# Kernel tuning notes

Measured on AMD Instinct MI355X. Metric: run time of the kernel, lower is better.

## Reference

```python
import jax, jax.numpy as jnp
import numpy as np

B = 16
TOP_N = 4
IOU_THRESH = 0.25
PAD = 224
OUT = 224  # part image size
NUM_CLASSES = 200


def _gen_anchors(input_shape=(448, 448)):
    # Faithful port of NTSNet._generate_default_anchor_maps -> edge anchors,
    # then +PAD shift and int cast as in NTSNet.__init__.
    scales = [2.0 ** (1.0 / 3.0), 2.0 ** (2.0 / 3.0)]
    ratios = [0.667, 1.0, 1.5]
    settings = [(32, 48, scales), (64, 96, scales), (128, 192, [1.0] + scales)]
    edge = []
    for stride, size, scs in settings:
        H = int(np.ceil(input_shape[0] / stride))
        W = int(np.ceil(input_shape[1] / stride))
        ostart = stride / 2.0
        oy = np.arange(ostart, ostart + stride * H, stride).reshape(H, 1)
        ox = np.arange(ostart, ostart + stride * W, stride).reshape(1, W)
        cy = np.broadcast_to(oy, (H, W)).astype(np.float32)
        cx = np.broadcast_to(ox, (H, W)).astype(np.float32)
        for s in scs:
            for ar in ratios:
                h = size * s / float(ar) ** 0.5
                w = size * s * float(ar) ** 0.5
                e = np.stack([cy - h / 2.0, cx - w / 2.0, cy + h / 2.0, cx + w / 2.0], axis=-1)
                edge.append(e.reshape(-1, 4))
    edge = np.concatenate(edge, axis=0).astype(np.float32)
    return (edge + PAD).astype(np.int64).astype(np.int32)  # [1614,4] (y0,x0,y1,x1)


def _conv(x, w, b, stride, pad):
    y = jax.lax.conv_general_dilated(
        x, w, window_strides=(stride, stride),
        padding=[(pad, pad), (pad, pad)],
        dimension_numbers=("NCHW", "OIHW", "NCHW"))
    return y + b[None, :, None, None]


def _nms_single(scores, boxes, areas):
    # Hard NMS, fixed TOP_N iterations (jit-friendly): iteratively take the
    # highest-score box and suppress boxes with IoU >= IOU_THRESH.
    valid = jnp.ones(scores.shape, dtype=bool)
    picked = []
    for _ in range(TOP_N):
        i = jnp.argmax(jnp.where(valid, scores, -jnp.inf))
        b = boxes[i]
        ih = jnp.minimum(boxes[:, 2], b[2]) - jnp.maximum(boxes[:, 0], b[0])
        iw = jnp.minimum(boxes[:, 3], b[3]) - jnp.maximum(boxes[:, 1], b[1])
        inter = jnp.where((ih < 0) | (iw < 0), 0.0, ih * iw)
        iou = inter / (areas + areas[i] - inter)
        valid = valid & (iou < IOU_THRESH)
        picked.append(i)
    return jnp.stack(picked)  # [TOP_N]


def _crop_resize(img, box):
    # Bilinear resize of img[:, y0:y1, x0:x1] to OUTxOUT, align_corners=True
    # (matches F.interpolate(..., mode='bilinear', align_corners=True)).
    y0, x0, y1, x1 = box[0], box[1], box[2], box[3]
    h = (y1 - y0).astype(jnp.float32)
    w = (x1 - x0).astype(jnp.float32)
    t = jnp.arange(OUT, dtype=jnp.float32)
    sy = t * (h - 1.0) / (OUT - 1.0)
    sx = t * (w - 1.0) / (OUT - 1.0)
    fy = jnp.floor(sy)
    fx = jnp.floor(sx)
    wy = (sy - fy)[None, :, None]  # broadcast over rows
    wx = (sx - fx)[None, None, :]  # broadcast over cols
    iy0 = y0 + fy.astype(jnp.int32)
    ix0 = x0 + fx.astype(jnp.int32)
    iy1 = jnp.minimum(iy0 + 1, y1 - 1)
    ix1 = jnp.minimum(ix0 + 1, x1 - 1)
    r0 = img[:, iy0]  # [3,OUT,896]
    r1 = img[:, iy1]
    top = r0[:, :, ix0] * (1.0 - wx) + r0[:, :, ix1] * wx
    bot = r1[:, :, ix0] * (1.0 - wx) + r1[:, :, ix1] * wx
    return top * (1.0 - wy) + bot * wy  # [3,OUT,OUT]


def setup_inputs() -> dict:
    key = jax.random.key(0)
    ks = jax.random.split(key, 10)
    s = 0.02
    inp = {
        "x": jax.random.normal(ks[0], (B, 3, 448, 448), jnp.float32),
        "bb_w": jax.random.normal(ks[1], (2048, 3, 32, 32), jnp.float32) * s,
        "bb_b": jnp.zeros((2048,), jnp.float32),
        "n1_dw": jax.random.normal(ks[2], (128, 2048, 3, 3), jnp.float32) * s,
        "n1_db": jnp.zeros((128,), jnp.float32),
        "n1_tw": jax.random.normal(ks[3], (6, 128, 1, 1), jnp.float32) * s,
        "n1_tb": jnp.zeros((6,), jnp.float32),
        "n2_dw": jax.random.normal(ks[4], (128, 128, 3, 3), jnp.float32) * s,
        "n2_db": jnp.zeros((128,), jnp.float32),
        "n2_tw": jax.random.normal(ks[5], (6, 128, 1, 1), jnp.float32) * s,
        "n2_tb": jnp.zeros((6,), jnp.float32),
        "n3_dw": jax.random.normal(ks[6], (128, 128, 3, 3), jnp.float32) * s,
        "n3_db": jnp.zeros((128,), jnp.float32),
        "n3_tw": jax.random.normal(ks[7], (9, 128, 1, 1), jnp.float32) * s,
        "n3_tb": jnp.zeros((9,), jnp.float32),
        "cn_w": jax.random.normal(ks[8], (NUM_CLASSES, 10240), jnp.float32) * s,
        "cn_b": jnp.zeros((NUM_CLASSES,), jnp.float32),
        "anchors": jnp.asarray(_gen_anchors()),
    }
    return inp


def reference(x, bb_w, bb_b, n1_dw, n1_db, n1_tw, n1_tb, n2_dw, n2_db, n2_tw,
              n2_tb, n3_dw, n3_db, n3_tw, n3_tb, cn_w, cn_b, anchors):
    batch = x.shape[0]
    # Backbone -> raw pre-features [B,2048,14,14]
    raw = _conv(x, bb_w, bb_b, stride=32, pad=0)
    # Navigator unit -> rpn scores [B,1614]
    y1 = jax.nn.relu(_conv(raw, n1_dw, n1_db, 1, 1))            # [B,128,14,14]
    t1 = _conv(y1, n1_tw, n1_tb, 1, 0).reshape(batch, -1)        # [B,1176]
    y2 = jax.nn.relu(_conv(y1, n2_dw, n2_db, 2, 1))              # [B,128,7,7]
    t2 = _conv(y2, n2_tw, n2_tb, 1, 0).reshape(batch, -1)        # [B,294]
    y3 = jax.nn.relu(_conv(y2, n3_dw, n3_db, 2, 1))              # [B,128,4,4]
    t3 = _conv(y3, n3_tw, n3_tb, 1, 0).reshape(batch, -1)        # [B,144]
    rpn_score = jnp.concatenate([t1, t2, t3], axis=1)            # [B,1614]

    boxes_f = anchors.astype(jnp.float32)
    areas = (boxes_f[:, 2] - boxes_f[:, 0]) * (boxes_f[:, 3] - boxes_f[:, 1])
    top_idx = jax.vmap(_nms_single, in_axes=(0, None, None))(rpn_score, boxes_f, areas)  # [B,TOP_N]

    x_pad = jnp.pad(x, ((0, 0), (0, 0), (PAD, PAD), (PAD, PAD)))  # [B,3,896,896]
    sel_boxes = anchors[top_idx]                                  # [B,TOP_N,4]
    part_imgs = jax.vmap(lambda img, bs: jax.vmap(_crop_resize, in_axes=(None, 0))(img, bs))(
        x_pad, sel_boxes)                                         # [B,TOP_N,3,224,224]
    part_imgs = jax.lax.stop_gradient(part_imgs).reshape(batch * TOP_N, 3, OUT, OUT)

    # Shared backbone + tail (global avg pool; dropout is identity in eval)
    part_features = _conv(part_imgs, bb_w, bb_b, 32, 0).mean(axis=(2, 3))  # [B*TOP_N,2048]
    part_feature = part_features.reshape(batch, TOP_N, -1)[:, :4].reshape(batch, -1)  # num_cat=4
    raw_features = jax.lax.stop_gradient(raw).mean(axis=(2, 3))            # [B,2048]

    concat_out = jnp.concatenate([part_feature, raw_features], axis=1)     # [B,10240]
    concat_logits = concat_out @ cn_w.T + cn_b
    return concat_logits
```

## Files before the change

### kernel.cpp

```cpp
#include <hip/hip_runtime.h>
#include <cstdint>
#include <math.h>

typedef _Float16 half_t;
typedef __attribute__((ext_vector_type(8))) _Float16 half8;
typedef __attribute__((ext_vector_type(4))) float floatx4;


typedef __attribute__((address_space(3))) unsigned int lds_u32;
typedef const __attribute__((address_space(1))) unsigned int glb_u32;
__device__ __forceinline__ void glds16(const void* g, void* l) {
    __builtin_amdgcn_global_load_lds((glb_u32*)g, (lds_u32*)l, 16, 0, 0);
}

__global__ __launch_bounds__(256)
void prep_all(const float* __restrict__ x, const float* __restrict__ bbw,
              const float* __restrict__ n1dw, const float* __restrict__ n2dw,
              const float* __restrict__ n3dw, const float* __restrict__ cnb,
              const float* __restrict__ bbb,
              half_t* __restrict__ xh,
              half_t* __restrict__ bh, half_t* __restrict__ w1h,
              float* __restrict__ wt2t, float* __restrict__ wt3t,
              float* __restrict__ out, float* __restrict__ zpad,
              float* __restrict__ concat)
{
    const int t = blockIdx.x * 256 + threadIdx.x;
    if (t < 307200) {
        const int m = t % 3200, s = t / 3200;
        const int mt = m >> 7, mr = m & 127;
        float f[32];
        if (m < 3136) {
            const int bq = m / 196, pos = m % 196, oy = pos / 14, ox = pos % 14;
            const int c = s >> 5, r = s & 31;
            const float* p = x + ((size_t)(bq * 3 + c) * 448 + oy * 32 + r) * 448 + ox * 32;
            #pragma unroll
            for (int i = 0; i < 8; ++i) *(float4*)&f[i * 4] = *(const float4*)(p + i * 4);
        } else {
            #pragma unroll
            for (int j = 0; j < 32; ++j) f[j] = 0.f;
        }
        #pragma unroll
        for (int kg = 0; kg < 4; ++kg) {
            half8 h;
            #pragma unroll
            for (int j = 0; j < 8; ++j) h[j] = (half_t)f[kg * 8 + j];
            const size_t dst = (((size_t)(mt * 96 + s) * 4 + kg) * 128 + mr) * 8;
            *(half8*)(xh + dst) = h;
        }
    } else if (t < 503808) {
        const int t2 = t - 307200;
        const int n = t2 & 2047, s = t2 >> 11;
        const float* p = bbw + (size_t)n * 3072 + s * 32;
        float f[32];
        #pragma unroll
        for (int i = 0; i < 8; ++i) *(float4*)&f[i * 4] = *(const float4*)(p + i * 4);
        const int nt = n >> 6, nr = n & 63;
        #pragma unroll
        for (int kg = 0; kg < 4; ++kg) {
            half8 h;
            #pragma unroll
            for (int j = 0; j < 8; ++j) h[j] = (half_t)f[kg * 8 + j];
            const size_t dst = (((size_t)(nt * 96 + s) * 4 + kg) * 64 + nr) * 8;
            *(half8*)(bh + dst) = h;
        }
    } else if (t < 536576) {
        const int t2 = t - 503808;
        const int n = t2 >> 8, ic8 = t2 & 255;
        const int s = ic8 >> 2, kg = ic8 & 3;
        const float* src = n1dw + ((size_t)n * 2048 + ic8 * 8) * 9;
        float buf[72];
        #pragma unroll
        for (int i = 0; i < 18; ++i) *(float4*)&buf[i * 4] = *(const float4*)(src + i * 4);
        #pragma unroll
        for (int tap = 0; tap < 9; ++tap) {
            half8 h;
            #pragma unroll
            for (int j = 0; j < 8; ++j) h[j] = (half_t)buf[j * 9 + tap];
            const size_t dst = (((size_t)(tap * 64 + s) * 4 + kg) * 128 + n) * 8;
            *(half8*)(w1h + dst) = h;
        }
    } else if (t < 684032) {
        const int t2 = t - 536576;
        const int oc = t2 % 128, rest = t2 / 128, ic = rest % 128, tap = rest / 128;
        wt2t[(tap * 128 + ic) * 128 + oc] = n2dw[((size_t)oc * 128 + ic) * 9 + tap];
    } else if (t < 831488) {
        const int t2 = t - 684032;
        const int oc = t2 % 128, rest = t2 / 128, ic = rest % 128, tap = rest / 128;
        wt3t[(tap * 128 + ic) * 128 + oc] = n3dw[((size_t)oc * 128 + ic) * 9 + tap];
    } else if (t < 834688) {
        const int i = t - 831488;
        out[i] = cnb[i % 200];
    } else if (t < 834944) {
        zpad[t - 834688] = 0.f;
    } else if (t < 998784) {
        const int i = t - 834944;
        const int r = i % 10240;
        concat[i] = (r < 8192) ? bbb[r & 2047] : 0.f;
    }
}

__global__ __launch_bounds__(256)
void gemm_x(const half_t* __restrict__ Ah, const half_t* __restrict__ Bh,
            const float* __restrict__ bias, half_t* __restrict__ outh)
{
    __shared__ __align__(16) char L[32768];
    const int tid = threadIdx.x, lane = tid & 63, wv = tid >> 6;
    const int nt = blockIdx.x, mt = blockIdx.y;
    const int lm = lane & 15, quad = lane >> 4;

    const char* pA = (const char*)Ah + (size_t)(mt >> 1) * 786432 + (mt & 1) * 1024
                   + quad * 2048 + (wv * 16 + lm) * 16;
    const char* gB = (const char*)Bh + (size_t)(2 * nt) * 393216 + lane * 16;

    const int bsi = wv >> 1, bnh = wv & 1;
    const size_t bgb = (size_t)bnh * 393216 + bsi * 4096;
    const int blb = (bsi * 2 + bnh) * 4096;

    floatx4 acc[8];
    const floatx4 fz = {0.f, 0.f, 0.f, 0.f};
    #pragma unroll
    for (int j = 0; j < 8; ++j) acc[j] = fz;

    half8 aC0, aC1, aN0, aN1;

    #pragma unroll
    for (int i = 0; i < 4; ++i)
        glds16(gB + bgb + i * 1024, L + blb + i * 1024);
    aC0 = *(const half8*)(pA);
    aC1 = *(const half8*)(pA + 8192);

    auto step = [&](int s, int sn, const char* Lc, char* Ln,
                    half8& c0, half8& c1, half8& n0, half8& n1) {
        #pragma unroll
        for (int i = 0; i < 4; ++i)
            glds16(gB + bgb + (size_t)sn * 8192 + i * 1024, Ln + blb + i * 1024);
        n0 = *(const half8*)(pA + (size_t)sn * 16384);
        n1 = *(const half8*)(pA + (size_t)sn * 16384 + 8192);
        asm volatile("s_waitcnt vmcnt(6)" ::: "memory");
        __builtin_amdgcn_s_barrier();
        __builtin_amdgcn_sched_barrier(0);
        #pragma unroll
        for (int ki = 0; ki < 2; ++ki) {
            const half8 a = ki ? c1 : c0;
            #pragma unroll
            for (int j = 0; j < 8; ++j) {
                half8 b = *(const half8*)(Lc + (ki * 2 + (j >> 2)) * 4096 + quad * 1024 + ((j & 3) * 16 + lm) * 16);
                acc[j] = __builtin_amdgcn_mfma_f32_16x16x32_f16(a, b, acc[j], 0, 0, 0);
            }
        }
        __builtin_amdgcn_sched_barrier(0);
        __builtin_amdgcn_s_barrier();
    };

    for (int h = 0; h < 24; ++h) {
        const int s0 = 2 * h, s1 = 2 * h + 1;
        step(s0, s0 + 1, L, L + 16384, aC0, aC1, aN0, aN1);
        step(s1, (s1 < 47) ? s1 + 1 : 0, L + 16384, L, aN0, aN1, aC0, aC1);
    }

    const int m0 = mt * 64 + wv * 16 + quad * 4;
    #pragma unroll
    for (int j = 0; j < 8; ++j) {
        const int n = nt * 128 + j * 16 + lm;
        const float bv = bias[n];
        #pragma unroll
        for (int r = 0; r < 4; ++r)
            outh[(size_t)(m0 + r) * 2048 + n] = (half_t)(acc[j][r] + bv);
    }
}

__global__ __launch_bounds__(256)
void gemm_nav(const half_t* __restrict__ rawh, const half_t* __restrict__ Bh,
              const char* __restrict__ zpad, float* __restrict__ y1p)
{
    __shared__ __align__(16) char L[32768];
    const int tid = threadIdx.x, lane = tid & 63, wv = tid >> 6;
    const int tx = blockIdx.x;
    const int tap = tx >> 1, ks = tx & 1;
    const int mt = blockIdx.y;
    const int lm = lane & 15, quad = lane >> 4;

    const int grow = mt * 64 + wv * 16 + lm;
    const int b = grow / 196, pos = grow % 196, oy = pos / 14, ox = pos % 14;
    const int iy = oy + tap / 3 - 1, ix = ox + tap % 3 - 1;
    const bool av = (iy >= 0 && iy < 14 && ix >= 0 && ix < 14);
    const char* fb = av ? (const char*)rawh + ((size_t)(b * 196 + iy * 14 + ix)) * 4096 + ks * 2048 : zpad;
    const int fstp = av ? 1 : 0;
    const char* fbase = fb + fstp * quad * 16;

    const int bsi = wv >> 1, bnh = wv & 1;
    const char* gB = (const char*)Bh + (size_t)tap * 524288 + (size_t)(ks * 32) * 8192 + bnh * 1024 + lane * 16;
    const int blb = bsi * 8192 + bnh * 1024;

    floatx4 acc[8];
    const floatx4 fz = {0.f, 0.f, 0.f, 0.f};
    #pragma unroll
    for (int j = 0; j < 8; ++j) acc[j] = fz;

    half8 aC0, aC1, aN0, aN1;

    #pragma unroll
    for (int i = 0; i < 4; ++i)
        glds16(gB + (size_t)bsi * 8192 + i * 2048, L + blb + i * 2048);
    aC0 = *(const half8*)(fbase);
    aC1 = *(const half8*)(fbase + fstp * 64);

    auto step = [&](int s, int sn, const char* Lc, char* Ln,
                    half8& c0, half8& c1, half8& n0, half8& n1) {
        #pragma unroll
        for (int i = 0; i < 4; ++i)
            glds16(gB + (size_t)(2 * sn + bsi) * 8192 + i * 2048, Ln + blb + i * 2048);
        n0 = *(const half8*)(fbase + fstp * (sn * 128));
        n1 = *(const half8*)(fbase + fstp * (sn * 128 + 64));
        asm volatile("s_waitcnt vmcnt(6)" ::: "memory");
        __builtin_amdgcn_s_barrier();
        __builtin_amdgcn_sched_barrier(0);
        #pragma unroll
        for (int ki = 0; ki < 2; ++ki) {
            const half8 a = ki ? c1 : c0;
            #pragma unroll
            for (int j = 0; j < 8; ++j) {
                half8 bq = *(const half8*)(Lc + ki * 8192 + quad * 2048 + (j * 16 + lm) * 16);
                acc[j] = __builtin_amdgcn_mfma_f32_16x16x32_f16(a, bq, acc[j], 0, 0, 0);
            }
        }
        __builtin_amdgcn_sched_barrier(0);
        __builtin_amdgcn_s_barrier();
    };

    for (int h = 0; h < 8; ++h) {
        const int s0 = 2 * h, s1 = 2 * h + 1;
        step(s0, s0 + 1, L, L + 16384, aC0, aC1, aN0, aN1);
        step(s1, (s1 < 15) ? s1 + 1 : 0, L + 16384, L, aN0, aN1, aC0, aC1);
    }

    const int m0 = mt * 64 + wv * 16 + quad * 4;
    #pragma unroll
    for (int j = 0; j < 8; ++j) {
        const int n = j * 16 + lm;
        #pragma unroll
        for (int r = 0; r < 4; ++r)
            y1p[((size_t)tx * 3136 + m0 + r) * 128 + n] = acc[j][r];
    }
}

__global__ __launch_bounds__(256)
void y1r_rm(const float* __restrict__ y1p, const float* __restrict__ bias,
            float* __restrict__ y1,
            const half_t* __restrict__ rh, float* __restrict__ concat)
{
    if (blockIdx.x < 1568) {
        const int t = blockIdx.x * 256 + threadIdx.x;
        const int n = t & 127;
        float s = bias[n];
        #pragma unroll
        for (int ks = 0; ks < 18; ++ks) s += y1p[(size_t)ks * 3136 * 128 + t];
        y1[t] = fmaxf(s, 0.f);
    } else {
        const int t = (blockIdx.x - 1568) * 256 + threadIdx.x;
        const int n = t & 2047, b = (t >> 11) & 15, pc = t >> 15;
        float s = 0.f;
        const int p0 = pc * 49;
        for (int p = p0; p < p0 + 49; ++p)
            s += (float)rh[(size_t)(b * 196 + p) * 2048 + n];
        atomicAdd(concat + (size_t)b * 10240 + 8192 + n, s * (1.f / 196.f));
    }
}

__device__ __forceinline__ void tidy_one(const float* in, const float* wr, float bi,
                                         float* dst, int lane)
{
    float acc = in[lane] * wr[lane] + in[lane + 64] * wr[lane + 64];
    #pragma unroll
    for (int s = 32; s > 0; s >>= 1) acc += __shfl_down(acc, s, 64);
    if (lane == 0) *dst = acc + bi;
}

__device__ __forceinline__ void conv_s2_body(int t, const float* __restrict__ in,
                                             const float* __restrict__ wt,
                                             const float* __restrict__ bias,
                                             float* __restrict__ out, int Win, int Wout)
{
    const int oc = t & 127;
    const int pos = (t >> 7) % (Wout * Wout);
    const int b = t / (128 * Wout * Wout);
    if (b >= 16) return;
    const int oy = pos / Wout, ox = pos % Wout;
    float acc = bias[oc];
    for (int dy = 0; dy < 3; ++dy) {
        const int y = oy * 2 + dy - 1;
        if (y < 0 || y >= Win) continue;
        for (int dx = 0; dx < 3; ++dx) {
            const int x = ox * 2 + dx - 1;
            if (x < 0 || x >= Win) continue;
            const float* ip = in + (size_t)(b * Win * Win + y * Win + x) * 128;
            const float* wp = wt + (size_t)(dy * 3 + dx) * 16384 + oc;
            for (int ic = 0; ic < 128; ++ic)
                acc += ip[ic] * wp[ic * 128];
        }
    }
    out[(size_t)(b * Wout * Wout + pos) * 128 + oc] = fmaxf(acc, 0.f);
}

__global__ __launch_bounds__(256)
void conv2_tidy1(const float* __restrict__ y1, const float* __restrict__ wt2t,
                 const float* __restrict__ b2d, float* __restrict__ y2,
                 const float* __restrict__ w1t, const float* __restrict__ b1t,
                 float* __restrict__ scores)
{
    if (blockIdx.x < 392) {
        conv_s2_body(blockIdx.x * 256 + threadIdx.x, y1, wt2t, b2d, y2, 14, 7);
    } else {
        const int wid = (blockIdx.x - 392) * 4 + (threadIdx.x >> 6);
        const int lane = threadIdx.x & 63;
        if (wid >= 16 * 1176) return;
        const int b = wid / 1176, i1 = wid % 1176;
        const int ch = i1 / 196, pos = i1 % 196;
        tidy_one(y1 + (size_t)(b * 196 + pos) * 128, w1t + ch * 128, b1t[ch],
                 scores + b * 1614 + i1, lane);
    }
}

__global__ __launch_bounds__(256)
void conv3_tidy2(const float* __restrict__ y2, const float* __restrict__ wt3t,
                 const float* __restrict__ b3d, float* __restrict__ y3,
                 const float* __restrict__ w2t, const float* __restrict__ b2t,
                 float* __restrict__ scores)
{
    if (blockIdx.x < 128) {
        conv_s2_body(blockIdx.x * 256 + threadIdx.x, y2, wt3t, b3d, y3, 7, 4);
    } else {
        const int wid = (blockIdx.x - 128) * 4 + (threadIdx.x >> 6);
        const int lane = threadIdx.x & 63;
        if (wid >= 16 * 294) return;
        const int b = wid / 294, i2 = wid % 294;
        const int ch = i2 / 49, pos = i2 % 49;
        tidy_one(y2 + (size_t)(b * 49 + pos) * 128, w2t + ch * 128, b2t[ch],
                 scores + b * 1614 + 1176 + i2, lane);
    }
}

__global__ __launch_bounds__(256)
void tidy3(const float* __restrict__ y3, const float* __restrict__ w3t,
           const float* __restrict__ b3t, float* __restrict__ scores)
{
    const int wid = blockIdx.x * 4 + (threadIdx.x >> 6);
    const int lane = threadIdx.x & 63;
    if (wid >= 16 * 144) return;
    const int b = wid / 144, i3 = wid % 144;
    const int ch = i3 / 16, pos = i3 % 16;
    tidy_one(y3 + (size_t)(b * 16 + pos) * 128, w3t + ch * 128, b3t[ch],
             scores + b * 1614 + 1470 + i3, lane);
}

__global__ __launch_bounds__(256)
void nms(const float* __restrict__ scores, const int* __restrict__ anchors,
         int* __restrict__ top_idx)
{
    __shared__ float wv_v[4];
    __shared__ int wv_i[4];
    __shared__ int s_pick;
    const int b = blockIdx.x, tid = threadIdx.x;
    const int lane = tid & 63, wv = tid >> 6;
    float sc[7], ay0[7], ax0[7], ay1[7], ax1[7];
    unsigned int vmask = 0;
    #pragma unroll
    for (int j = 0; j < 7; ++j) {
        const int i = tid + j * 256;
        if (i < 1614) {
            sc[j]  = scores[b * 1614 + i];
            ay0[j] = (float)anchors[i * 4 + 0];
            ax0[j] = (float)anchors[i * 4 + 1];
            ay1[j] = (float)anchors[i * 4 + 2];
            ax1[j] = (float)anchors[i * 4 + 3];
            vmask |= 1u << j;
        }
    }
    for (int r = 0; r < 4; ++r) {
        float bv = -INFINITY; int bi = 0x7fffffff;
        #pragma unroll
        for (int j = 0; j < 7; ++j) {
            if (vmask & (1u << j)) {
                const float v = sc[j];
                const int i = tid + j * 256;
                if (v > bv || (v == bv && i < bi)) { bv = v; bi = i; }
            }
        }
        #pragma unroll
        for (int s = 32; s > 0; s >>= 1) {
            const float v2 = __shfl_down(bv, s, 64);
            const int   i2 = __shfl_down(bi, s, 64);
            if (v2 > bv || (v2 == bv && i2 < bi)) { bv = v2; bi = i2; }
        }
        if (lane == 0) { wv_v[wv] = bv; wv_i[wv] = bi; }
        __syncthreads();
        if (tid == 0) {
            float fv = wv_v[0]; int fi = wv_i[0];
            #pragma unroll
            for (int k = 1; k < 4; ++k)
                if (wv_v[k] > fv || (wv_v[k] == fv && wv_i[k] < fi)) { fv = wv_v[k]; fi = wv_i[k]; }
            s_pick = fi;
            top_idx[b * 4 + r] = fi;
        }
        __syncthreads();
        const int pick = s_pick;
        const float py0 = (float)anchors[pick * 4 + 0], px0 = (float)anchors[pick * 4 + 1];
        const float py1 = (float)anchors[pick * 4 + 2], px1 = (float)anchors[pick * 4 + 3];
        const float pa = (py1 - py0) * (px1 - px0);
        #pragma unroll
        for (int j = 0; j < 7; ++j) {
            if (vmask & (1u << j)) {
                const float ih = fminf(ay1[j], py1) - fmaxf(ay0[j], py0);
                const float iw = fminf(ax1[j], px1) - fmaxf(ax0[j], px0);
                const float inter = (ih < 0.f || iw < 0.f) ? 0.f : ih * iw;
                const float area = (ay1[j] - ay0[j]) * (ax1[j] - ax0[j]);
                const float iou = inter / ((area + pa) - inter);
                if (iou >= 0.25f) vmask &= ~(1u << j);
            }
        }
    }
}

__global__ __launch_bounds__(256)
void crop_mean(const float* __restrict__ x, const int* __restrict__ anchors,
               const int* __restrict__ top_idx, float* __restrict__ abar)
{
    __shared__ float red[256];
    const int bi = blockIdx.x;
    const int q = bi / 96, rem = bi % 96, c = rem >> 5, r = rem & 31;
    const int tid = threadIdx.x;
    const int cc = tid & 31, ps = tid >> 5;
    const int idx = top_idx[q];
    const int y0 = anchors[idx * 4 + 0], x0 = anchors[idx * 4 + 1];
    const int y1 = anchors[idx * 4 + 2], x1 = anchors[idx * 4 + 3];
    const float hh = (float)(y1 - y0), ww = (float)(x1 - x0);
    const float* xb = x + (size_t)((q >> 2) * 3 + c) * 200704;
    float acc = 0.f;
    for (int p = ps; p < 49; p += 8) {
        const int oy = p / 7, ox = p % 7;
        const int typ = oy * 32 + r;
        const int txp = ox * 32 + cc;
        const float sy = (float)typ * (hh - 1.0f) / 223.0f;
        const float fy = floorf(sy);
        const float wy = sy - fy;
        const int iy0 = y0 + (int)fy;
        const int iy1 = min(iy0 + 1, y1 - 1);
        const float sx = (float)txp * (ww - 1.0f) / 223.0f;
        const float fx = floorf(sx);
        const float wx = sx - fx;
        const int ix0 = x0 + (int)fx;
        const int ix1 = min(ix0 + 1, x1 - 1);
        const int ry0 = iy0 - 224, ry1 = iy1 - 224;
        const int rx0 = ix0 - 224, rx1 = ix1 - 224;
        const bool vy0 = (ry0 >= 0 && ry0 < 448), vy1 = (ry1 >= 0 && ry1 < 448);
        const bool vx0 = (rx0 >= 0 && rx0 < 448), vx1 = (rx1 >= 0 && rx1 < 448);
        const float v00 = (vy0 && vx0) ? xb[(size_t)ry0 * 448 + rx0] : 0.f;
        const float v01 = (vy0 && vx1) ? xb[(size_t)ry0 * 448 + rx1] : 0.f;
        const float v10 = (vy1 && vx0) ? xb[(size_t)ry1 * 448 + rx0] : 0.f;
        const float v11 = (vy1 && vx1) ? xb[(size_t)ry1 * 448 + rx1] : 0.f;
        const float top = v00 * (1.f - wx) + v01 * wx;
        const float bot = v10 * (1.f - wx) + v11 * wx;
        acc += top * (1.f - wy) + bot * wy;
    }
    red[tid] = acc;
    __syncthreads();
    if (tid < 32) {
        float s = 0.f;
        #pragma unroll
        for (int k = 0; k < 8; ++k) s += red[tid + 32 * k];
        abar[(size_t)q * 3072 + c * 1024 + r * 32 + cc] = s * (1.f / 49.f);
    }
}

__global__ __launch_bounds__(256)
void part_gemm(const float* __restrict__ abar, const half_t* __restrict__ Bh,
               float* __restrict__ concat)
{
    __shared__ __align__(16) char L[12288];
    const int tid = threadIdx.x, lane = tid & 63, wv = tid >> 6;
    const int lm = lane & 15, quad = lane >> 4;
    const int nt = blockIdx.x, ks = blockIdx.y;
    const char* gBh = (const char*)Bh + ((size_t)nt * 96 + ks * 12) * 4096 + lane * 16;
    const int am = tid & 63, akg = tid >> 6;

    floatx4 acc[4], accl[4];
    const floatx4 fz = {0.f, 0.f, 0.f, 0.f};
    #pragma unroll
    for (int j = 0; j < 4; ++j) { acc[j] = fz; accl[j] = fz; }

    for (int s = 0; s < 12; ++s) {
        {
            const float* pa = abar + (size_t)am * 3072 + (ks * 12 + s) * 32 + akg * 8;
            float f[8];
            *(float4*)&f[0] = *(const float4*)pa;
            *(float4*)&f[4] = *(const float4*)(pa + 4);
            half8 h, l;
            #pragma unroll
            for (int j = 0; j < 8; ++j) {
                const half_t hh = (half_t)f[j];
                h[j] = hh;
                l[j] = (half_t)(f[j] - (float)hh);
            }
            *(half8*)(L + (akg * 64 + am) * 16) = h;
            *(half8*)(L + 4096 + (akg * 64 + am) * 16) = l;
        }
        glds16(gBh + (size_t)s * 4096 + wv * 1024, L + 8192 + wv * 1024);
        __syncthreads();
        half8 ah, al, bh[4];
        ah = *(const half8*)(L + (quad * 64 + wv * 16 + lm) * 16);
        al = *(const half8*)(L + 4096 + (quad * 64 + wv * 16 + lm) * 16);
        #pragma unroll
        for (int j = 0; j < 4; ++j) bh[j] = *(const half8*)(L + 8192 + (quad * 64 + j * 16 + lm) * 16);
        #pragma unroll
        for (int j = 0; j < 4; ++j) {
            acc[j]  = __builtin_amdgcn_mfma_f32_16x16x32_f16(ah, bh[j], acc[j], 0, 0, 0);
            accl[j] = __builtin_amdgcn_mfma_f32_16x16x32_f16(al, bh[j], accl[j], 0, 0, 0);
        }
        __syncthreads();
    }
    #pragma unroll
    for (int j = 0; j < 4; ++j) {
        const int n = nt * 64 + j * 16 + lm;
        #pragma unroll
        for (int r = 0; r < 4; ++r) {
            const int m = wv * 16 + quad * 4 + r;
            atomicAdd(concat + (size_t)(m >> 2) * 10240 + (m & 3) * 2048 + n,
                      acc[j][r] + accl[j][r]);
        }
    }
}

__global__ __launch_bounds__(256)
void cls_gemm(const float* __restrict__ concat, const float* __restrict__ w,
              float* __restrict__ out)
{
    __shared__ float ws_[8 * 321];
    __shared__ float cs_[16 * 321];
    __shared__ float red[256];
    const int nchunk = blockIdx.x, ks = blockIdx.y;
    const int tid = threadIdx.x;
    for (int i = tid; i < 2560; i += 256) {
        const int r = i / 320, k = i % 320;
        ws_[r * 321 + k] = w[(size_t)(nchunk * 8 + r) * 10240 + ks * 320 + k];
    }
    for (int i = tid; i < 5120; i += 256) {
        const int r = i / 320, k = i % 320;
        cs_[r * 321 + k] = concat[(size_t)r * 10240 + ks * 320 + k];
    }
    __syncthreads();
    const int b = tid & 15, c = (tid >> 4) & 7, hf = tid >> 7;
    const float* cp = cs_ + b * 321 + hf * 160;
    const float* wp = ws_ + c * 321 + hf * 160;
    float a = 0.f;
    #pragma unroll 8
    for (int k = 0; k < 160; ++k) a += cp[k] * wp[k];
    red[tid] = a;
    __syncthreads();
    if (tid < 128) atomicAdd(out + b * 200 + nchunk * 8 + c, red[tid] + red[tid + 128]);
}

extern "C" void kernel_launch(void* const* d_in, const int* in_sizes, int n_in,
                              void* d_out, int out_size, void* d_ws, size_t ws_size,
                              hipStream_t stream)
{
    const float* x     = (const float*)d_in[0];
    const float* bb_w  = (const float*)d_in[1];
    const float* bb_b  = (const float*)d_in[2];
    const float* n1_dw = (const float*)d_in[3];
    const float* n1_db = (const float*)d_in[4];
    const float* n1_tw = (const float*)d_in[5];
    const float* n1_tb = (const float*)d_in[6];
    const float* n2_dw = (const float*)d_in[7];
    const float* n2_db = (const float*)d_in[8];
    const float* n2_tw = (const float*)d_in[9];
    const float* n2_tb = (const float*)d_in[10];
    const float* n3_dw = (const float*)d_in[11];
    const float* n3_db = (const float*)d_in[12];
    const float* n3_tw = (const float*)d_in[13];
    const float* n3_tb = (const float*)d_in[14];
    const float* cn_w  = (const float*)d_in[15];
    const float* cn_b  = (const float*)d_in[16];
    const int*   anchors = (const int*)d_in[17];
    float* out = (float*)d_out;
    char* W = (char*)d_ws;

    half_t* bbwh  = (half_t*)(W + 0);
    float*  zpad  = (float*)(W + 12582912);
    int*    topidx= (int*)(W + 12583936);
    float*  scores= (float*)(W + 12584960);
    float*  y1    = (float*)(W + 12688384);
    float*  y2    = (float*)(W + 14294016);
    float*  y3    = (float*)(W + 14695424);
    float*  concat= (float*)(W + 14826496);
    half_t* w1h   = (half_t*)(W + 15481856);
    float*  wt2t  = (float*)(W + 20200448);
    float*  wt3t  = (float*)(W + 20790272);
    char* E = W + 21380096;
    half_t* xh    = (half_t*)E;
    float*  y1p   = (float*)E;
    char* F = W + 60701696;
    half_t* rawh  = (half_t*)F;
    float*  abar  = (float*)F;

    prep_all<<<3902, 256, 0, stream>>>(x, bb_w, n1_dw, n2_dw, n3_dw, cn_b, bb_b,
                                       xh, bbwh, w1h, wt2t, wt3t, out, zpad, concat);

    gemm_x<<<dim3(16, 49), 256, 0, stream>>>(xh, bbwh, bb_b, rawh);
    gemm_nav<<<dim3(18, 49), 256, 0, stream>>>(rawh, w1h, (const char*)zpad, y1p);
    y1r_rm<<<2080, 256, 0, stream>>>(y1p, n1_db, y1, rawh, concat);

    conv2_tidy1<<<5096, 256, 0, stream>>>(y1, wt2t, n2_db, y2, n1_tw, n1_tb, scores);
    conv3_tidy2<<<1304, 256, 0, stream>>>(y2, wt3t, n3_db, y3, n2_tw, n2_tb, scores);
    tidy3<<<576, 256, 0, stream>>>(y3, n3_tw, n3_tb, scores);

    nms<<<16, 256, 0, stream>>>(scores, anchors, topidx);
    crop_mean<<<6144, 256, 0, stream>>>(x, anchors, topidx, abar);

    part_gemm<<<dim3(32, 8), 256, 0, stream>>>(abar, bbwh, concat);
    cls_gemm<<<dim3(25, 32), 256, 0, stream>>>(concat, cn_w, out);
}
```

Baseline: 380.5 us.

## Switch backbone and navigator GEMMs to 32x32x16 MFMA with 2x2 wave tiling

Both the feature GEMM and the navigator conv GEMM move from 16x16x32 MFMA with each wave owning 16 rows by 128 columns to 32x32x16 MFMA with a 2x2 wave grid, each wave owning a 32x64 output tile. This cuts LDS reads of B per MFMA and reduces the MFMA instruction count for the same work. The cost is four A fragments in flight per step instead of two, an adjusted vmcnt wait, and a new output-store index mapping that must match the 32x32 accumulator layout.

```diff
diff --git a/kernel.cpp b/kernel.cpp
--- a/kernel.cpp
+++ b/kernel.cpp
@@ -5,6 +5,7 @@
 typedef _Float16 half_t;
 typedef __attribute__((ext_vector_type(8))) _Float16 half8;
 typedef __attribute__((ext_vector_type(4))) float floatx4;
+typedef __attribute__((ext_vector_type(16))) float floatx16;
 
 
 typedef __attribute__((address_space(3))) unsigned int lds_u32;
@@ -105,67 +106,78 @@
 {
     __shared__ __align__(16) char L[32768];
     const int tid = threadIdx.x, lane = tid & 63, wv = tid >> 6;
-    const int nt = blockIdx.x, mt = blockIdx.y;
-    const int lm = lane & 15, quad = lane >> 4;
-
-    const char* pA = (const char*)Ah + (size_t)(mt >> 1) * 786432 + (mt & 1) * 1024
-                   + quad * 2048 + (wv * 16 + lm) * 16;
+    const int nt = blockIdx.x, mt2 = blockIdx.y;
+    const int l31 = lane & 31, hi = lane >> 5;
+    const int wr = wv >> 1, wc = wv & 1;
+
+    const int mr = (mt2 & 1) * 64 + wr * 32 + l31;
+    const char* gA = (const char*)Ah + (size_t)(mt2 >> 1) * 786432 + (size_t)hi * 2048 + mr * 16;
+
     const char* gB = (const char*)Bh + (size_t)(2 * nt) * 393216 + lane * 16;
-
     const int bsi = wv >> 1, bnh = wv & 1;
     const size_t bgb = (size_t)bnh * 393216 + bsi * 4096;
     const int blb = (bsi * 2 + bnh) * 4096;
 
-    floatx4 acc[8];
-    const floatx4 fz = {0.f, 0.f, 0.f, 0.f};
-    #pragma unroll
-    for (int j = 0; j < 8; ++j) acc[j] = fz;
-
-    half8 aC0, aC1, aN0, aN1;
+    const int brd = wc * 4096 + hi * 1024 + l31 * 16;
+
+    floatx16 acc0 = {0.f}, acc1 = {0.f};
+    #pragma unroll
+    for (int r = 0; r < 16; ++r) { acc0[r] = 0.f; acc1[r] = 0.f; }
+
+    half8 aC0, aC1, aC2, aC3, aN0, aN1, aN2, aN3;
 
     #pragma unroll
     for (int i = 0; i < 4; ++i)
         glds16(gB + bgb + i * 1024, L + blb + i * 1024);
-    aC0 = *(const half8*)(pA);
-    aC1 = *(const half8*)(pA + 8192);
-
-    auto step = [&](int s, int sn, const char* Lc, char* Ln,
-                    half8& c0, half8& c1, half8& n0, half8& n1) {
+    aC0 = *(const half8*)(gA);
+    aC1 = *(const half8*)(gA + 4096);
+    aC2 = *(const half8*)(gA + 8192);
+    aC3 = *(const half8*)(gA + 12288);
+
+    auto step = [&](int sn, const char* Lc, char* Ln,
+                    half8& c0, half8& c1, half8& c2, half8& c3,
+                    half8& n0, half8& n1, half8& n2, half8& n3) {
         #pragma unroll
         for (int i = 0; i < 4; ++i)
             glds16(gB + bgb + (size_t)sn * 8192 + i * 1024, Ln + blb + i * 1024);
-        n0 = *(const half8*)(pA + (size_t)sn * 16384);
-        n1 = *(const half8*)(pA + (size_t)sn * 16384 + 8192);
-        asm volatile("s_waitcnt vmcnt(6)" ::: "memory");
+        const char* pAs = gA + (size_t)sn * 16384;
+        n0 = *(const half8*)(pAs);
+        n1 = *(const half8*)(pAs + 4096);
+        n2 = *(const half8*)(pAs + 8192);
+        n3 = *(const half8*)(pAs + 12288);
+        asm volatile("s_waitcnt vmcnt(8)" ::: "memory");
         __builtin_amdgcn_s_barrier();
         __builtin_amdgcn_sched_barrier(0);
         #pragma unroll
-        for (int ki = 0; ki < 2; ++ki) {
-            const half8 a = ki ? c1 : c0;
-            #pragma unroll
-            for (int j = 0; j < 8; ++j) {
-                half8 b = *(const half8*)(Lc + (ki * 2 + (j >> 2)) * 4096 + quad * 1024 + ((j & 3) * 16 + lm) * 16);
-                acc[j] = __builtin_amdgcn_mfma_f32_16x16x32_f16(a, b, acc[j], 0, 0, 0);
-            }
+        for (int t = 0; t < 4; ++t) {
+            const half8 a = (t == 0) ? c0 : (t == 1) ? c1 : (t == 2) ? c2 : c3;
+            const char* bb = Lc + (t >> 1) * 8192 + (t & 1) * 2048 + brd;
+            half8 b0 = *(const half8*)(bb);
+            half8 b1 = *(const half8*)(bb + 512);
+            acc0 = __builtin_amdgcn_mfma_f32_32x32x16_f16(a, b0, acc0, 0, 0, 0);
+            acc1 = __builtin_amdgcn_mfma_f32_32x32x16_f16(a, b1, acc1, 0, 0, 0);
         }
         __builtin_amdgcn_sched_barrier(0);
         __builtin_amdgcn_s_barrier();
     };
 
     for (int h = 0; h < 24; ++h) {
-        const int s0 = 2 * h, s1 = 2 * h + 1;
-        step(s0, s0 + 1, L, L + 16384, aC0, aC1, aN0, aN1);
-        step(s1, (s1 < 47) ? s1 + 1 : 0, L + 16384, L, aN0, aN1, aC0, aC1);
-    }
-
-    const int m0 = mt * 64 + wv * 16 + quad * 4;
-    #pragma unroll
-    for (int j = 0; j < 8; ++j) {
-        const int n = nt * 128 + j * 16 + lm;
+        const int s1 = 2 * h + 1;
+        step(s1, L, L + 16384, aC0, aC1, aC2, aC3, aN0, aN1, aN2, aN3);
+        step((s1 < 47) ? s1 + 1 : 0, L + 16384, L, aN0, aN1, aN2, aN3, aC0, aC1, aC2, aC3);
+    }
+
+    const int m0 = mt2 * 64 + wr * 32 + 4 * hi;
+    #pragma unroll
+    for (int c = 0; c < 2; ++c) {
+        const int n = nt * 128 + wc * 64 + c * 32 + l31;
         const float bv = bias[n];
-        #pragma unroll
-        for (int r = 0; r < 4; ++r)
-            outh[(size_t)(m0 + r) * 2048 + n] = (half_t)(acc[j][r] + bv);
+        const floatx16 av = c ? acc1 : acc0;
+        #pragma unroll
+        for (int r = 0; r < 16; ++r) {
+            const int row = m0 + (r & 3) + 8 * (r >> 2);
+            outh[(size_t)row * 2048 + n] = (half_t)(av[r] + bv);
+        }
     }
 }
 
@@ -178,69 +190,80 @@
     const int tx = blockIdx.x;
     const int tap = tx >> 1, ks = tx & 1;
     const int mt = blockIdx.y;
-    const int lm = lane & 15, quad = lane >> 4;
-
-    const int grow = mt * 64 + wv * 16 + lm;
+    const int l31 = lane & 31, hi = lane >> 5;
+    const int wr = wv >> 1, wc = wv & 1;
+
+    const int grow = mt * 64 + wr * 32 + l31;
     const int b = grow / 196, pos = grow % 196, oy = pos / 14, ox = pos % 14;
     const int iy = oy + tap / 3 - 1, ix = ox + tap % 3 - 1;
     const bool av = (iy >= 0 && iy < 14 && ix >= 0 && ix < 14);
     const char* fb = av ? (const char*)rawh + ((size_t)(b * 196 + iy * 14 + ix)) * 4096 + ks * 2048 : zpad;
     const int fstp = av ? 1 : 0;
-    const char* fbase = fb + fstp * quad * 16;
+    const char* fbase = fb + fstp * (hi * 16);
 
     const int bsi = wv >> 1, bnh = wv & 1;
     const char* gB = (const char*)Bh + (size_t)tap * 524288 + (size_t)(ks * 32) * 8192 + bnh * 1024 + lane * 16;
     const int blb = bsi * 8192 + bnh * 1024;
 
-    floatx4 acc[8];
-    const floatx4 fz = {0.f, 0.f, 0.f, 0.f};
-    #pragma unroll
-    for (int j = 0; j < 8; ++j) acc[j] = fz;
-
-    half8 aC0, aC1, aN0, aN1;
+    const int brd = hi * 2048 + wc * 1024 + l31 * 16;
+
+    floatx16 acc0, acc1;
+    #pragma unroll
+    for (int r = 0; r < 16; ++r) { acc0[r] = 0.f; acc1[r] = 0.f; }
+
+    half8 aC0, aC1, aC2, aC3, aN0, aN1, aN2, aN3;
 
     #pragma unroll
     for (int i = 0; i < 4; ++i)
         glds16(gB + (size_t)bsi * 8192 + i * 2048, L + blb + i * 2048);
     aC0 = *(const half8*)(fbase);
-    aC1 = *(const half8*)(fbase + fstp * 64);
-
-    auto step = [&](int s, int sn, const char* Lc, char* Ln,
-                    half8& c0, half8& c1, half8& n0, half8& n1) {
+    aC1 = *(const half8*)(fbase + fstp * 32);
+    aC2 = *(const half8*)(fbase + fstp * 64);
+    aC3 = *(const half8*)(fbase + fstp * 96);
+
+    auto step = [&](int sn, const char* Lc, char* Ln,
+                    half8& c0, half8& c1, half8& c2, half8& c3,
+                    half8& n0, half8& n1, half8& n2, half8& n3) {
         #pragma unroll
         for (int i = 0; i < 4; ++i)
             glds16(gB + (size_t)(2 * sn + bsi) * 8192 + i * 2048, Ln + blb + i * 2048);
-        n0 = *(const half8*)(fbase + fstp * (sn * 128));
-        n1 = *(const half8*)(fbase + fstp * (sn * 128 + 64));
-        asm volatile("s_waitcnt vmcnt(6)" ::: "memory");
+        const char* pAs = fbase + fstp * (sn * 128);
+        n0 = *(const half8*)(pAs);
+        n1 = *(const half8*)(pAs + fstp * 32);
+        n2 = *(const half8*)(pAs + fstp * 64);
+        n3 = *(const half8*)(pAs + fstp * 96);
+        asm volatile("s_waitcnt vmcnt(8)" ::: "memory");
         __builtin_amdgcn_s_barrier();
         __builtin_amdgcn_sched_barrier(0);
         #pragma unroll
-        for (int ki = 0; ki < 2; ++ki) {
-            const half8 a = ki ? c1 : c0;
-            #pragma unroll
-            for (int j = 0; j < 8; ++j) {
-                half8 bq = *(const half8*)(Lc + ki * 8192 + quad * 2048 + (j * 16 + lm) * 16);
-                acc[j] = __builtin_amdgcn_mfma_f32_16x16x32_f16(a, bq, acc[j], 0, 0, 0);
-            }
+        for (int t = 0; t < 4; ++t) {
+            const half8 a = (t == 0) ? c0 : (t == 1) ? c1 : (t == 2) ? c2 : c3;
+            const char* bb = Lc + (t >> 1) * 8192 + (t & 1) * 4096 + brd;
+            half8 b0 = *(const half8*)(bb);
+            half8 b1 = *(const half8*)(bb + 512);
+            acc0 = __builtin_amdgcn_mfma_f32_32x32x16_f16(a, b0, acc0, 0, 0, 0);
+            acc1 = __builtin_amdgcn_mfma_f32_32x32x16_f16(a, b1, acc1, 0, 0, 0);
         }
         __builtin_amdgcn_sched_barrier(0);
         __builtin_amdgcn_s_barrier();
     };
 
     for (int h = 0; h < 8; ++h) {
-        const int s0 = 2 * h, s1 = 2 * h + 1;
-        step(s0, s0 + 1, L, L + 16384, aC0, aC1, aN0, aN1);
-        step(s1, (s1 < 15) ? s1 + 1 : 0, L + 16384, L, aN0, aN1, aC0, aC1);
-    }
-
-    const int m0 = mt * 64 + wv * 16 + quad * 4;
-    #pragma unroll
-    for (int j = 0; j < 8; ++j) {
-        const int n = j * 16 + lm;
-        #pragma unroll
-        for (int r = 0; r < 4; ++r)
-            y1p[((size_t)tx * 3136 + m0 + r) * 128 + n] = acc[j][r];
+        const int s1 = 2 * h + 1;
+        step(s1, L, L + 16384, aC0, aC1, aC2, aC3, aN0, aN1, aN2, aN3);
+        step((s1 < 15) ? s1 + 1 : 0, L + 16384, L, aN0, aN1, aN2, aN3, aC0, aC1, aC2, aC3);
+    }
+
+    const int m0 = mt * 64 + wr * 32 + 4 * hi;
+    #pragma unroll
+    for (int c = 0; c < 2; ++c) {
+        const int n = wc * 64 + c * 32 + l31;
+        const floatx16 avv = c ? acc1 : acc0;
+        #pragma unroll
+        for (int r = 0; r < 16; ++r) {
+            const int row = m0 + (r & 3) + 8 * (r >> 2);
+            y1p[((size_t)tx * 3136 + row) * 128 + n] = avv[r];
+        }
     }
 }
 
```

Result: slower. 401.6 us (+5.5%).

## Use two-wave blocks with 32-row per-wave tiles in backbone and nav GEMMs

Applied to the files above, without the earlier changes.

Both MFMA GEMM kernels now launch 128 threads instead of 256. Each wave computes two 16-row M subtiles against the same B fragments read from LDS, so every LDS B load feeds two MFMAs. Each wave now issues 8 global-to-LDS copies per step and 4 A-register loads, with the waitcnt adjusted to match. This raises per-wave register use and halves the waves per block, which may reduce latency hiding and occupancy while cutting LDS read traffic per MFMA.

```diff
diff --git a/kernel.cpp b/kernel.cpp
--- a/kernel.cpp
+++ b/kernel.cpp
@@ -99,7 +99,7 @@
     }
 }
 
-__global__ __launch_bounds__(256)
+__global__ __launch_bounds__(128)
 void gemm_x(const half_t* __restrict__ Ah, const half_t* __restrict__ Bh,
             const float* __restrict__ bias, half_t* __restrict__ outh)
 {
@@ -108,44 +108,52 @@
     const int nt = blockIdx.x, mt = blockIdx.y;
     const int lm = lane & 15, quad = lane >> 4;
 
-    const char* pA = (const char*)Ah + (size_t)(mt >> 1) * 786432 + (mt & 1) * 1024
-                   + quad * 2048 + (wv * 16 + lm) * 16;
+    const char* pA = (const char*)Ah + (size_t)(mt >> 1) * 786432
+                   + quad * 2048 + ((mt & 1) * 64 + wv * 32 + lm) * 16;
     const char* gB = (const char*)Bh + (size_t)(2 * nt) * 393216 + lane * 16;
 
-    const int bsi = wv >> 1, bnh = wv & 1;
-    const size_t bgb = (size_t)bnh * 393216 + bsi * 4096;
-    const int blb = (bsi * 2 + bnh) * 4096;
-
-    floatx4 acc[8];
+    floatx4 acc[2][8];
     const floatx4 fz = {0.f, 0.f, 0.f, 0.f};
     #pragma unroll
-    for (int j = 0; j < 8; ++j) acc[j] = fz;
-
-    half8 aC0, aC1, aN0, aN1;
-
-    #pragma unroll
-    for (int i = 0; i < 4; ++i)
-        glds16(gB + bgb + i * 1024, L + blb + i * 1024);
-    aC0 = *(const half8*)(pA);
-    aC1 = *(const half8*)(pA + 8192);
-
-    auto step = [&](int s, int sn, const char* Lc, char* Ln,
-                    half8& c0, half8& c1, half8& n0, half8& n1) {
-        #pragma unroll
-        for (int i = 0; i < 4; ++i)
-            glds16(gB + bgb + (size_t)sn * 8192 + i * 1024, Ln + blb + i * 1024);
-        n0 = *(const half8*)(pA + (size_t)sn * 16384);
-        n1 = *(const half8*)(pA + (size_t)sn * 16384 + 8192);
-        asm volatile("s_waitcnt vmcnt(6)" ::: "memory");
+    for (int mi = 0; mi < 2; ++mi)
+        #pragma unroll
+        for (int j = 0; j < 8; ++j) acc[mi][j] = fz;
+
+    half8 c0, c1, c2, c3, n0, n1, n2, n3;
+
+    #pragma unroll
+    for (int i = 0; i < 8; ++i)
+        glds16(gB + (size_t)(i >> 2) * 393216 + (size_t)wv * 4096 + (i & 3) * 1024,
+               L + wv * 8192 + i * 1024);
+    c0 = *(const half8*)(pA);
+    c1 = *(const half8*)(pA + 8192);
+    c2 = *(const half8*)(pA + 256);
+    c3 = *(const half8*)(pA + 8192 + 256);
+
+    auto step = [&](int sn, const char* Lc, char* Ln,
+                    half8& a00, half8& a01, half8& a10, half8& a11,
+                    half8& b00, half8& b01, half8& b10, half8& b11) {
+        #pragma unroll
+        for (int i = 0; i < 8; ++i)
+            glds16(gB + (size_t)(i >> 2) * 393216 + (size_t)(2 * sn + wv) * 4096 + (i & 3) * 1024,
+                   Ln + wv * 8192 + i * 1024);
+        const char* pAs = pA + (size_t)(2 * sn) * 8192;
+        b00 = *(const half8*)(pAs);
+        b01 = *(const half8*)(pAs + 8192);
+        b10 = *(const half8*)(pAs + 256);
+        b11 = *(const half8*)(pAs + 8192 + 256);
+        asm volatile("s_waitcnt vmcnt(12)" ::: "memory");
         __builtin_amdgcn_s_barrier();
         __builtin_amdgcn_sched_barrier(0);
         #pragma unroll
         for (int ki = 0; ki < 2; ++ki) {
-            const half8 a = ki ? c1 : c0;
+            const half8 a0 = ki ? a01 : a00;
+            const half8 a1 = ki ? a11 : a10;
             #pragma unroll
             for (int j = 0; j < 8; ++j) {
-                half8 b = *(const half8*)(Lc + (ki * 2 + (j >> 2)) * 4096 + quad * 1024 + ((j & 3) * 16 + lm) * 16);
-                acc[j] = __builtin_amdgcn_mfma_f32_16x16x32_f16(a, b, acc[j], 0, 0, 0);
+                half8 b = *(const half8*)(Lc + ki * 8192 + (j >> 2) * 4096 + quad * 1024 + ((j & 3) * 16 + lm) * 16);
+                acc[0][j] = __builtin_amdgcn_mfma_f32_16x16x32_f16(a0, b, acc[0][j], 0, 0, 0);
+                acc[1][j] = __builtin_amdgcn_mfma_f32_16x16x32_f16(a1, b, acc[1][j], 0, 0, 0);
             }
         }
         __builtin_amdgcn_sched_barrier(0);
@@ -153,23 +161,26 @@
     };
 
     for (int h = 0; h < 24; ++h) {
-        const int s0 = 2 * h, s1 = 2 * h + 1;
-        step(s0, s0 + 1, L, L + 16384, aC0, aC1, aN0, aN1);
-        step(s1, (s1 < 47) ? s1 + 1 : 0, L + 16384, L, aN0, aN1, aC0, aC1);
-    }
-
-    const int m0 = mt * 64 + wv * 16 + quad * 4;
+        const int s1 = 2 * h + 1;
+        step(s1, L, L + 16384, c0, c1, c2, c3, n0, n1, n2, n3);
+        step((s1 < 47) ? s1 + 1 : 0, L + 16384, L, n0, n1, n2, n3, c0, c1, c2, c3);
+    }
+
     #pragma unroll
     for (int j = 0; j < 8; ++j) {
         const int n = nt * 128 + j * 16 + lm;
         const float bv = bias[n];
         #pragma unroll
-        for (int r = 0; r < 4; ++r)
-            outh[(size_t)(m0 + r) * 2048 + n] = (half_t)(acc[j][r] + bv);
-    }
-}
-
-__global__ __launch_bounds__(256)
+        for (int mi = 0; mi < 2; ++mi) {
+            const int m0 = mt * 64 + wv * 32 + mi * 16 + quad * 4;
+            #pragma unroll
+            for (int r = 0; r < 4; ++r)
+                outh[(size_t)(m0 + r) * 2048 + n] = (half_t)(acc[mi][j][r] + bv);
+        }
+    }
+}
+
+__global__ __launch_bounds__(128)
 void gemm_nav(const half_t* __restrict__ rawh, const half_t* __restrict__ Bh,
               const char* __restrict__ zpad, float* __restrict__ y1p)
 {
@@ -180,48 +191,65 @@
     const int mt = blockIdx.y;
     const int lm = lane & 15, quad = lane >> 4;
 
-    const int grow = mt * 64 + wv * 16 + lm;
-    const int b = grow / 196, pos = grow % 196, oy = pos / 14, ox = pos % 14;
-    const int iy = oy + tap / 3 - 1, ix = ox + tap % 3 - 1;
-    const bool av = (iy >= 0 && iy < 14 && ix >= 0 && ix < 14);
-    const char* fb = av ? (const char*)rawh + ((size_t)(b * 196 + iy * 14 + ix)) * 4096 + ks * 2048 : zpad;
-    const int fstp = av ? 1 : 0;
-    const char* fbase = fb + fstp * quad * 16;
-
-    const int bsi = wv >> 1, bnh = wv & 1;
-    const char* gB = (const char*)Bh + (size_t)tap * 524288 + (size_t)(ks * 32) * 8192 + bnh * 1024 + lane * 16;
-    const int blb = bsi * 8192 + bnh * 1024;
-
-    floatx4 acc[8];
+    const char* fb0; const char* fb1; int fs0, fs1;
+    {
+        const int g0 = mt * 64 + wv * 32 + lm;
+        const int b = g0 / 196, pos = g0 % 196, oy = pos / 14, ox = pos % 14;
+        const int iy = oy + tap / 3 - 1, ix = ox + tap % 3 - 1;
+        const bool av = (iy >= 0 && iy < 14 && ix >= 0 && ix < 14);
+        fb0 = av ? (const char*)rawh + ((size_t)(b * 196 + iy * 14 + ix)) * 4096 + ks * 2048 : zpad;
+        fs0 = av ? 1 : 0;
+    }
+    {
+        const int g1 = mt * 64 + wv * 32 + 16 + lm;
+        const int b = g1 / 196, pos = g1 % 196, oy = pos / 14, ox = pos % 14;
+        const int iy = oy + tap / 3 - 1, ix = ox + tap % 3 - 1;
+        const bool av = (iy >= 0 && iy < 14 && ix >= 0 && ix < 14);
+        fb1 = av ? (const char*)rawh + ((size_t)(b * 196 + iy * 14 + ix)) * 4096 + ks * 2048 : zpad;
+        fs1 = av ? 1 : 0;
+    }
+
+    const char* gB = (const char*)Bh + (size_t)tap * 524288 + (size_t)(ks * 32) * 8192 + lane * 16;
+
+    floatx4 acc[2][8];
     const floatx4 fz = {0.f, 0.f, 0.f, 0.f};
     #pragma unroll
-    for (int j = 0; j < 8; ++j) acc[j] = fz;
-
-    half8 aC0, aC1, aN0, aN1;
-
-    #pragma unroll
-    for (int i = 0; i < 4; ++i)
-        glds16(gB + (size_t)bsi * 8192 + i * 2048, L + blb + i * 2048);
-    aC0 = *(const half8*)(fbase);
-    aC1 = *(const half8*)(fbase + fstp * 64);
-
-    auto step = [&](int s, int sn, const char* Lc, char* Ln,
-                    half8& c0, half8& c1, half8& n0, half8& n1) {
-        #pragma unroll
-        for (int i = 0; i < 4; ++i)
-            glds16(gB + (size_t)(2 * sn + bsi) * 8192 + i * 2048, Ln + blb + i * 2048);
-        n0 = *(const half8*)(fbase + fstp * (sn * 128));
-        n1 = *(const half8*)(fbase + fstp * (sn * 128 + 64));
-        asm volatile("s_waitcnt vmcnt(6)" ::: "memory");
+    for (int mi = 0; mi < 2; ++mi)
+        #pragma unroll
+        for (int j = 0; j < 8; ++j) acc[mi][j] = fz;
+
+    half8 c0, c1, c2, c3, n0, n1, n2, n3;
+
+    #pragma unroll
+    for (int i = 0; i < 8; ++i)
+        glds16(gB + (size_t)wv * 8192 + i * 1024, L + wv * 8192 + i * 1024);
+    c0 = *(const half8*)(fb0 + fs0 * (quad * 16));
+    c1 = *(const half8*)(fb0 + fs0 * (64 + quad * 16));
+    c2 = *(const half8*)(fb1 + fs1 * (quad * 16));
+    c3 = *(const half8*)(fb1 + fs1 * (64 + quad * 16));
+
+    auto step = [&](int sn, const char* Lc, char* Ln,
+                    half8& a00, half8& a01, half8& a10, half8& a11,
+                    half8& b00, half8& b01, half8& b10, half8& b11) {
+        #pragma unroll
+        for (int i = 0; i < 8; ++i)
+            glds16(gB + (size_t)(2 * sn + wv) * 8192 + i * 1024, Ln + wv * 8192 + i * 1024);
+        b00 = *(const half8*)(fb0 + fs0 * (sn * 128 + quad * 16));
+        b01 = *(const half8*)(fb0 + fs0 * (sn * 128 + 64 + quad * 16));
+        b10 = *(const half8*)(fb1 + fs1 * (sn * 128 + quad * 16));
+        b11 = *(const half8*)(fb1 + fs1 * (sn * 128 + 64 + quad * 16));
+        asm volatile("s_waitcnt vmcnt(12)" ::: "memory");
         __builtin_amdgcn_s_barrier();
         __builtin_amdgcn_sched_barrier(0);
         #pragma unroll
         for (int ki = 0; ki < 2; ++ki) {
-            const half8 a = ki ? c1 : c0;
+            const half8 a0 = ki ? a01 : a00;
+            const half8 a1 = ki ? a11 : a10;
             #pragma unroll
             for (int j = 0; j < 8; ++j) {
-                half8 bq = *(const half8*)(Lc + ki * 8192 + quad * 2048 + (j * 16 + lm) * 16);
-                acc[j] = __builtin_amdgcn_mfma_f32_16x16x32_f16(a, bq, acc[j], 0, 0, 0);
+                half8 b = *(const half8*)(Lc + ki * 8192 + quad * 2048 + (j * 16 + lm) * 16);
+                acc[0][j] = __builtin_amdgcn_mfma_f32_16x16x32_f16(a0, b, acc[0][j], 0, 0, 0);
+                acc[1][j] = __builtin_amdgcn_mfma_f32_16x16x32_f16(a1, b, acc[1][j], 0, 0, 0);
             }
         }
         __builtin_amdgcn_sched_barrier(0);
@@ -229,18 +257,21 @@
     };
 
     for (int h = 0; h < 8; ++h) {
-        const int s0 = 2 * h, s1 = 2 * h + 1;
-        step(s0, s0 + 1, L, L + 16384, aC0, aC1, aN0, aN1);
-        step(s1, (s1 < 15) ? s1 + 1 : 0, L + 16384, L, aN0, aN1, aC0, aC1);
-    }
-
-    const int m0 = mt * 64 + wv * 16 + quad * 4;
+        const int s1 = 2 * h + 1;
+        step(s1, L, L + 16384, c0, c1, c2, c3, n0, n1, n2, n3);
+        step((s1 < 15) ? s1 + 1 : 0, L + 16384, L, n0, n1, n2, n3, c0, c1, c2, c3);
+    }
+
     #pragma unroll
     for (int j = 0; j < 8; ++j) {
         const int n = j * 16 + lm;
         #pragma unroll
-        for (int r = 0; r < 4; ++r)
-            y1p[((size_t)tx * 3136 + m0 + r) * 128 + n] = acc[j][r];
+        for (int mi = 0; mi < 2; ++mi) {
+            const int m0 = mt * 64 + wv * 32 + mi * 16 + quad * 4;
+            #pragma unroll
+            for (int r = 0; r < 4; ++r)
+                y1p[((size_t)tx * 3136 + m0 + r) * 128 + n] = acc[mi][j][r];
+        }
     }
 }
 
@@ -605,8 +636,8 @@
     prep_all<<<3902, 256, 0, stream>>>(x, bb_w, n1_dw, n2_dw, n3_dw, cn_b, bb_b,
                                        xh, bbwh, w1h, wt2t, wt3t, out, zpad, concat);
 
-    gemm_x<<<dim3(16, 49), 256, 0, stream>>>(xh, bbwh, bb_b, rawh);
-    gemm_nav<<<dim3(18, 49), 256, 0, stream>>>(rawh, w1h, (const char*)zpad, y1p);
+    gemm_x<<<dim3(16, 49), 128, 0, stream>>>(xh, bbwh, bb_b, rawh);
+    gemm_nav<<<dim3(18, 49), 128, 0, stream>>>(rawh, w1h, (const char*)zpad, y1p);
     y1r_rm<<<2080, 256, 0, stream>>>(y1p, n1_db, y1, rawh, concat);
 
     conv2_tidy1<<<5096, 256, 0, stream>>>(y1, wt2t, n2_db, y2, n1_tw, n1_tb, scores);
```

Result: faster. 372.2 us (-2.2%).
